# Kernel optimization log

Measured on AMD Instinct MI355X. Metric: run time of the kernel, lower is better.

Reference implementation:

```python
import jax, jax.numpy as jnp
import numpy as np

BS, S, DM, H, DK, DV, PRED = 64, 128, 512, 8, 512, 512, 96
NF = S * DM  # Flatten_Head nf = patch_num * d_model
SCALE_INIT = (DM // H) ** (-0.5)  # head_dim from d_model//n_heads per _ScaledDotProductAttention


def setup_inputs() -> dict:
    key = jax.random.key(0)
    ks = jax.random.split(key, 24)
    g = lambda k, shp: (0.02 * jax.random.normal(k, shp)).astype(jnp.float32)
    inp = {
        "x": jax.random.normal(ks[0], (BS, S, DM), dtype=jnp.float32),
        "prev": jax.random.normal(ks[1], (BS, H, S, S), dtype=jnp.float32),
        # multi-head attention projections (d_k = d_v = d_model per TMBlock)
        "Wq": g(ks[2], (DM, H * DK)), "bq": jnp.zeros((H * DK,), jnp.float32),
        "Wk": g(ks[3], (DM, H * DK)), "bk": jnp.zeros((H * DK,), jnp.float32),
        "Wv": g(ks[4], (DM, H * DV)), "bv": jnp.zeros((H * DV,), jnp.float32),
        "Wo": g(ks[5], (H * DV, DM)), "bo": jnp.zeros((DM,), jnp.float32),
        "scale": jnp.float32(SCALE_INIT),
        # InterPatchMixing: Linear(PatchNum, PatchNum) x2
        "Wi1": g(ks[6], (S, S)), "bi1": jnp.zeros((S,), jnp.float32),
        "Wi2": g(ks[7], (S, S)), "bi2": jnp.zeros((S,), jnp.float32),
        # IntraPatchMixing: Linear(PatchEmbedDim, PatchEmbedDim) x2
        "Wt1": g(ks[8], (DM, DM)), "bt1": jnp.zeros((DM,), jnp.float32),
        "Wt2": g(ks[9], (DM, DM)), "bt2": jnp.zeros((DM,), jnp.float32),
        # Flatten_Head (non-individual): Linear(nf, pred_len)
        "Wh": g(ks[10], (NF, PRED)), "bh": jnp.zeros((PRED,), jnp.float32),
    }
    return inp


def reference(x, prev, Wq, bq, Wk, bk, Wv, bv, Wo, bo, scale,
              Wi1, bi1, Wi2, bi2, Wt1, bt1, Wt2, bt2, Wh, bh):
    bs = x.shape[0]
    # projections -> [bs, H, S, d]
    q = (x @ Wq + bq).reshape(bs, S, H, DK).transpose(0, 2, 1, 3)
    k = (x @ Wk + bk).reshape(bs, S, H, DK).transpose(0, 2, 1, 3)
    v = (x @ Wv + bv).reshape(bs, S, H, DV).transpose(0, 2, 1, 3)
    # manual scaled dot-product attention with residual attention bias (Realformer)
    scores = jnp.einsum('bhqd,bhkd->bhqk', q, k) * scale + prev
    attn = jax.nn.softmax(scores, axis=-1)  # dropout is identity at eval
    o = jnp.einsum('bhqk,bhkd->bhqd', attn, v)
    o = o.transpose(0, 2, 1, 3).reshape(bs, S, H * DV)
    o = o @ Wo + bo  # [bs, S, DM]
    # InterPatchMixing over the patch axis (last dim must be PatchNum)
    t = o.transpose(0, 2, 1)  # [bs, DM, S]
    t = jax.nn.relu(t @ Wi1 + bi1) @ Wi2 + bi2
    y = t.transpose(0, 2, 1)  # [bs, S, DM]
    # IntraPatchMixing over embed dim
    z = jax.nn.relu(y @ Wt1 + bt1) @ Wt2 + bt2
    # Flatten_Head: flatten last two dims -> Linear(nf, pred_len)
    out = z.reshape(bs, NF) @ Wh + bh  # [bs, PRED]
    return out
```

## Files before the change

kernel.cpp:

```cpp
#include <hip/hip_runtime.h>
#include <cstdint>
#include <cstddef>

typedef __bf16 bf16_t;
typedef __bf16 bf16x8 __attribute__((ext_vector_type(8)));
typedef __bf16 bf16x4 __attribute__((ext_vector_type(4)));
typedef float  f32x4  __attribute__((ext_vector_type(4)));

#define MFMA(a, b, c) __builtin_amdgcn_mfma_f32_16x16x32_bf16((a), (b), (c), 0, 0, 0)

__device__ __forceinline__ void gload16(const bf16_t* g, bf16_t* l) {
  __builtin_amdgcn_global_load_lds(
      (const __attribute__((address_space(1))) void*)g,
      (__attribute__((address_space(3))) void*)l, 16, 0, 0);
}


__global__ __launch_bounds__(256) void k_convert_dual(const float* __restrict__ in,
                                                      bf16_t* __restrict__ xb,
                                                      bf16_t* __restrict__ xT) {
  __shared__ bf16_t tile[32][34];
  int tx = threadIdx.x & 31, ty = threadIdx.x >> 5;
  int c0 = blockIdx.x * 32, r0 = blockIdx.y * 32;
#pragma unroll
  for (int j = 0; j < 4; ++j) {
    int r = r0 + ty + j * 8;
    bf16_t bv = (bf16_t)in[(size_t)r * 512 + c0 + tx];
    xb[(size_t)r * 512 + c0 + tx] = bv;
    tile[ty + j * 8][tx] = bv;
  }
  __syncthreads();
  int b = (r0 + tx) >> 7, s = (r0 + tx) & 127;
#pragma unroll
  for (int j = 0; j < 4; ++j) {
    int i = c0 + ty + j * 8;
    xT[(size_t)b * 65536 + (size_t)i * 128 + s] = tile[tx][ty + j * 8];
  }
}

__global__ __launch_bounds__(256) void k_transpose_convert(const float* __restrict__ in,
                                                           bf16_t* __restrict__ out,
                                                           int R, int C) {
  __shared__ float tile[32][33];
  int tx = threadIdx.x & 31, ty = threadIdx.x >> 5;
  int c0 = blockIdx.x * 32, r0 = blockIdx.y * 32;
#pragma unroll
  for (int j = 0; j < 4; ++j)
    tile[ty + j * 8][tx] = in[(size_t)(r0 + ty + j * 8) * C + c0 + tx];
  __syncthreads();
#pragma unroll
  for (int j = 0; j < 4; ++j)
    out[(size_t)(c0 + ty + j * 8) * R + r0 + tx] = (bf16_t)tile[tx][ty + j * 8];
}

__global__ __launch_bounds__(256) void k_transpose_b16(const bf16_t* __restrict__ in,
                                                       bf16_t* __restrict__ out,
                                                       int R, int C) {
  __shared__ bf16_t tile[32][34];
  size_t base = (size_t)blockIdx.z * R * C;
  int tx = threadIdx.x & 31, ty = threadIdx.x >> 5;
  int c0 = blockIdx.x * 32, r0 = blockIdx.y * 32;
#pragma unroll
  for (int j = 0; j < 4; ++j)
    tile[ty + j * 8][tx] = in[base + (size_t)(r0 + ty + j * 8) * C + c0 + tx];
  __syncthreads();
#pragma unroll
  for (int j = 0; j < 4; ++j)
    out[base + (size_t)(c0 + ty + j * 8) * R + r0 + tx] = tile[tx][ty + j * 8];
}

template <int BMODE>
__global__ __launch_bounds__(256) void k_wprod(const float* __restrict__ Ap,
                                               const float* __restrict__ Bp,
                                               bf16_t* __restrict__ out,
                                               int ldA, int ldB) {
  __shared__ __align__(16) bf16_t S[128 * 68 * 2];
  bf16_t* As = S;
  bf16_t* Bs = S + 128 * 68;
  const int tid = threadIdx.x, lane = tid & 63, wave = tid >> 6;
  const int wr = (wave >> 1) * 64, wc = (wave & 1) * 64;
  const int lr = lane & 15, lk = (lane >> 4) * 8, frow = (lane >> 4) * 4;
  const int m0 = blockIdx.x * 128, n0 = blockIdx.y * 128, h = blockIdx.z;
  const int sr = tid >> 3, sc = (tid & 7) * 8;
  f32x4 acc[4][4] = {};

  for (int kt = 0; kt < 512; kt += 64) {
#pragma unroll
    for (int rr = 0; rr < 4; ++rr) {
      int r = sr + 32 * rr;
      const float* ap = Ap + (size_t)(m0 + r) * ldA + h * 512 + kt + sc;
      bf16x8 av;
#pragma unroll
      for (int e = 0; e < 8; ++e) av[e] = (bf16_t)ap[e];
      *(bf16x8*)(As + r * 68 + sc) = av;
    }
    if (BMODE == 0) {
#pragma unroll
      for (int rr = 0; rr < 4; ++rr) {
        int r = sr + 32 * rr;
        const float* bp = Bp + (size_t)(n0 + r) * ldB + h * 512 + kt + sc;
        bf16x8 bv;
#pragma unroll
        for (int e = 0; e < 8; ++e) bv[e] = (bf16_t)bp[e];
        *(bf16x8*)(Bs + r * 68 + sc) = bv;
      }
    } else {
#pragma unroll
      for (int rr = 0; rr < 8; ++rr) {
        int kr = (tid >> 5) + 8 * rr;
        int nc = (tid & 31) * 4;
        const float* bp = Bp + (size_t)(h * 512 + kt + kr) * ldB + n0 + nc;
        float4 v = *(const float4*)bp;
        Bs[(nc + 0) * 68 + kr] = (bf16_t)v.x;
        Bs[(nc + 1) * 68 + kr] = (bf16_t)v.y;
        Bs[(nc + 2) * 68 + kr] = (bf16_t)v.z;
        Bs[(nc + 3) * 68 + kr] = (bf16_t)v.w;
      }
    }
    __syncthreads();
#pragma unroll
    for (int kk = 0; kk < 2; ++kk) {
      bf16x8 af[4], bfr[4];
#pragma unroll
      for (int i = 0; i < 4; ++i)
        af[i] = *(const bf16x8*)(As + (wr + i * 16 + lr) * 68 + kk * 32 + lk);
#pragma unroll
      for (int j = 0; j < 4; ++j)
        bfr[j] = *(const bf16x8*)(Bs + (wc + j * 16 + lr) * 68 + kk * 32 + lk);
#pragma unroll
      for (int i = 0; i < 4; ++i)
#pragma unroll
        for (int j = 0; j < 4; ++j)
          acc[i][j] = MFMA(af[i], bfr[j], acc[i][j]);
    }
    __syncthreads();
  }

  bf16_t* Full = S;
#pragma unroll
  for (int i = 0; i < 4; ++i)
#pragma unroll
    for (int j = 0; j < 4; ++j)
#pragma unroll
      for (int q = 0; q < 4; ++q)
        Full[(wc + j * 16 + lr) * 136 + wr + i * 16 + frow + q] = (bf16_t)acc[i][j][q];
  __syncthreads();
#pragma unroll
  for (int it = 0; it < 8; ++it) {
    int r = it * 16 + (tid >> 4);
    int c = (tid & 15) * 8;
    *(bf16x8*)(out + ((size_t)(h * 512 + n0 + r)) * 512 + m0 + c) =
        *(const bf16x8*)(Full + r * 136 + c);
  }
}

__global__ __launch_bounds__(256) void k_sbias2(const float* __restrict__ Wq,
                                                const float* __restrict__ bk,
                                                const float* __restrict__ Wk,
                                                const float* __restrict__ bq,
                                                bf16_t* __restrict__ W12b,
                                                float* __restrict__ c) {
  const int lane = threadIdx.x & 63, wave = threadIdx.x >> 6;
  const int i = blockIdx.x * 4 + wave;
  for (int h = 0; h < 8; ++h) {
    float s1 = 0.f, s2 = 0.f;
    for (int d = lane; d < 512; d += 64) {
      s1 += Wq[(size_t)i * 4096 + h * 512 + d] * bk[h * 512 + d];
      s2 += Wk[(size_t)i * 4096 + h * 512 + d] * bq[h * 512 + d];
    }
#pragma unroll
    for (int o = 32; o > 0; o >>= 1) { s1 += __shfl_down(s1, o); s2 += __shfl_down(s2, o); }
    if (lane == 0) {
      W12b[h * 512 + i] = (bf16_t)s1;
      W12b[(8 + h) * 512 + i] = (bf16_t)s2;
    }
  }
  if (blockIdx.x == 0 && wave == 0) {
    for (int h = 0; h < 8; ++h) {
      float cc = 0.f;
      for (int d = lane; d < 512; d += 64) cc += bq[h * 512 + d] * bk[h * 512 + d];
#pragma unroll
      for (int o = 32; o > 0; o >>= 1) cc += __shfl_down(cc, o);
      if (lane == 0) c[h] = cc;
    }
  }
}

__global__ __launch_bounds__(256) void k_tbias2(const bf16_t* __restrict__ xb,
                                                const bf16_t* __restrict__ W12b,
                                                const float* __restrict__ cb,
                                                float* __restrict__ TallT) {
  __shared__ __align__(16) bf16_t Ws[16 * 516];
  const int tid = threadIdx.x, lane = tid & 63, wave = tid >> 6;
  const int lr = lane & 15, lk = (lane >> 4) * 8, frow = (lane >> 4) * 4;
  for (int i = tid; i < 1024; i += 256) {
    int r = i >> 6, ccol = (i & 63) * 8;
    *(bf16x8*)(Ws + r * 516 + ccol) = *(const bf16x8*)(W12b + r * 512 + ccol);
  }
  __syncthreads();
  const int row0 = blockIdx.x * 64 + wave * 16;
  const bf16_t* xr = xb + (size_t)(row0 + lr) * 512 + lk;
  f32x4 acc = {};
#pragma unroll
  for (int kx = 0; kx < 16; ++kx) {
    bf16x8 af = *(const bf16x8*)(xr + kx * 32);
    bf16x8 bfv = *(const bf16x8*)(Ws + lr * 516 + kx * 32 + lk);
    acc = MFMA(af, bfv, acc);
  }
#pragma unroll
  for (int q = 0; q < 4; ++q) {
    int r = row0 + frow + q;
    float v = acc[q] + (lr < 8 ? cb[lr] : 0.f);
    TallT[(size_t)lr * 8192 + r] = v;
  }
}

__global__ __launch_bounds__(256) void k_cvec1(const float* __restrict__ bv,
                                               const float* __restrict__ Wo,
                                               float* __restrict__ cpart) {
  int cch = blockIdx.x, d = threadIdx.x * 2;
  float ax = 0.f, ay = 0.f;
  for (int n = cch * 128; n < cch * 128 + 128; ++n) {
    float b = bv[n];
    float2 w = *(const float2*)(Wo + (size_t)n * 512 + d);
    ax += b * w.x; ay += b * w.y;
  }
  cpart[(size_t)cch * 512 + d] = ax;
  cpart[(size_t)cch * 512 + d + 1] = ay;
}
__global__ __launch_bounds__(256) void k_cvec2(const float* __restrict__ cpart,
                                               const float* __restrict__ bo,
                                               float* __restrict__ cvec) {
  int d = blockIdx.x * 256 + threadIdx.x;
  float s = bo[d];
  for (int cch = 0; cch < 32; ++cch) s += cpart[(size_t)cch * 512 + d];
  cvec[d] = s;
}

__global__ __launch_bounds__(64, 2) void k_attn9(const bf16_t* __restrict__ xb,
                                                 const bf16_t* __restrict__ xT,
                                                 bf16_t* __restrict__ TU,
                                                 const float* __restrict__ prev,
                                                 const float* __restrict__ scale_p,
                                                 const float* __restrict__ TallT,
                                                 int hg) {
  __shared__ __align__(16) bf16_t Pl[16 * 136];
  __shared__ __align__(16) bf16_t Bw[16 * 72];

  const int lane = threadIdx.x;
  const int lr = lane & 15, lk = (lane >> 4) * 8, frow = (lane >> 4) * 4;
  const int bid = blockIdx.x;
  const int bx = (bid & 7) * 256 + (bid >> 3);
  const int b = bx >> 5, hp = (bx >> 3) & 3, rg = bx & 7;
  const int h = hg * 4 + hp;
  const int r0 = rg * 16;
  const bf16_t* xB = xb + (size_t)b * 65536;
  const bf16_t* xTB = xT + (size_t)b * 65536;
  bf16_t* tB = TU + ((size_t)hp * 8192 + b * 128 + r0) * 512;

  bf16x8 tf[16];
  const bf16_t* aP = tB + (size_t)lr * 512 + lk;
#pragma unroll
  for (int kx = 0; kx < 16; ++kx) tf[kx] = *(const bf16x8*)(aP + kx * 32);

  f32x4 sacc[8] = {};
  const bf16_t* bP = xB + (size_t)lr * 512 + lk;
#pragma unroll
  for (int kc = 0; kc < 8; ++kc) {
    bf16x8 bb0[8], bb1[8];
#pragma unroll
    for (int j = 0; j < 8; ++j)
      bb0[j] = *(const bf16x8*)(bP + (size_t)j * 8192 + (2 * kc) * 32);
#pragma unroll
    for (int j = 0; j < 8; ++j)
      bb1[j] = *(const bf16x8*)(bP + (size_t)j * 8192 + (2 * kc + 1) * 32);
    __builtin_amdgcn_s_setprio(1);
#pragma unroll
    for (int j = 0; j < 8; ++j) sacc[j] = MFMA(tf[2 * kc], bb0[j], sacc[j]);
#pragma unroll
    for (int j = 0; j < 8; ++j) sacc[j] = MFMA(tf[2 * kc + 1], bb1[j], sacc[j]);
    __builtin_amdgcn_s_setprio(0);
  }

  const float scl = scale_p[0];
  const float* t1p = TallT + h * 8192 + b * 128 + r0;
  const float* t2p = TallT + (8 + h) * 8192 + b * 128;
  float t2r[8];
#pragma unroll
  for (int j = 0; j < 8; ++j) t2r[j] = t2p[j * 16 + lr];
#pragma unroll
  for (int e = 0; e < 4; ++e) {
    const int rl = frow + e;
    const float t1 = t1p[rl];
    const float* prow = prev + (((size_t)(b * 8 + h)) * 128 + r0 + rl) * 128;
    float pv[8];
#pragma unroll
    for (int j = 0; j < 8; ++j) pv[j] = prow[j * 16 + lr];
    float mx = -3.4e38f;
#pragma unroll
    for (int j = 0; j < 8; ++j) {
      float v = scl * (sacc[j][e] + t1 + t2r[j]) + pv[j];
      sacc[j][e] = v;
      mx = fmaxf(mx, v);
    }
    mx = fmaxf(mx, __shfl_xor(mx, 1));
    mx = fmaxf(mx, __shfl_xor(mx, 2));
    mx = fmaxf(mx, __shfl_xor(mx, 4));
    mx = fmaxf(mx, __shfl_xor(mx, 8));
    float sum = 0.f;
#pragma unroll
    for (int j = 0; j < 8; ++j) {
      float p = __expf(sacc[j][e] - mx);
      sacc[j][e] = p;
      sum += p;
    }
    sum += __shfl_xor(sum, 1);
    sum += __shfl_xor(sum, 2);
    sum += __shfl_xor(sum, 4);
    sum += __shfl_xor(sum, 8);
    float inv = 1.f / sum;
#pragma unroll
    for (int j = 0; j < 8; ++j)
      Pl[rl * 136 + j * 16 + lr] = (bf16_t)(sacc[j][e] * inv);
  }

#pragma unroll
  for (int dc = 0; dc < 8; ++dc) {
    bf16x8 xf[16];
#pragma unroll
    for (int kk = 0; kk < 4; ++kk)
#pragma unroll
      for (int j = 0; j < 4; ++j)
        xf[kk * 4 + j] =
            *(const bf16x8*)(xTB + (size_t)(dc * 64 + j * 16 + lr) * 128 + kk * 32 + lk);
    f32x4 oacc[4] = {};
    __builtin_amdgcn_s_setprio(1);
#pragma unroll
    for (int kk = 0; kk < 4; ++kk) {
      bf16x8 pa = *(const bf16x8*)(Pl + lr * 136 + kk * 32 + lk);
#pragma unroll
      for (int j = 0; j < 4; ++j) oacc[j] = MFMA(pa, xf[kk * 4 + j], oacc[j]);
    }
    __builtin_amdgcn_s_setprio(0);
#pragma unroll
    for (int j = 0; j < 4; ++j)
#pragma unroll
      for (int e = 0; e < 4; ++e)
        Bw[(frow + e) * 72 + j * 16 + lr] = (bf16_t)oacc[j][e];
#pragma unroll
    for (int r2 = 0; r2 < 2; ++r2) {
      int row = lane >> 2, chunk = (lane & 3) + r2 * 4;
      *(bf16x8*)(tB + (size_t)row * 512 + dc * 64 + chunk * 8) =
          *(const bf16x8*)(Bw + row * 72 + chunk * 8);
    }
  }
}

template <int OUTMODE, int RELU>
__global__ __launch_bounds__(256) void k_gemm(const bf16_t* __restrict__ A,
                                              const bf16_t* __restrict__ Bt,
                                              const float* __restrict__ bias,
                                              bf16_t* __restrict__ C,
                                              int M, int N, int K) {
  __shared__ __align__(16) bf16_t As[128 * 64];
  __shared__ __align__(16) bf16_t Bs[128 * 64];
  const int tid = threadIdx.x, lane = tid & 63, wave = tid >> 6;
  const int wr = (wave >> 1) * 64, wc = (wave & 1) * 64;
  const int m0 = blockIdx.x * 128, n0 = blockIdx.y * 128;
  const int lr = lane & 15, lk = (lane >> 4) * 8, frow = (lane >> 4) * 4;
  const int grow = lane >> 3;
  const int gcol = ((lane & 7) ^ grow) * 8;
  const int rmask = (lr & 7) << 3;
  f32x4 acc[4][4] = {};

  for (int kt = 0; kt < K; kt += 64) {
#pragma unroll
    for (int i = 0; i < 4; ++i) {
      int t = wave * 4 + i;
      int row = t * 8 + grow;
      gload16(A + (size_t)(m0 + row) * K + kt + gcol, As + t * 512);
      gload16(Bt + (size_t)(n0 + row) * K + kt + gcol, Bs + t * 512);
    }
    __syncthreads();
#pragma unroll
    for (int kk = 0; kk < 2; ++kk) {
      const int col = (kk * 32 + lk) ^ rmask;
      bf16x8 af[4], bfr[4];
#pragma unroll
      for (int i = 0; i < 4; ++i)
        af[i] = *(const bf16x8*)(As + (wr + i * 16 + lr) * 64 + col);
#pragma unroll
      for (int j = 0; j < 4; ++j)
        bfr[j] = *(const bf16x8*)(Bs + (wc + j * 16 + lr) * 64 + col);
#pragma unroll
      for (int i = 0; i < 4; ++i)
#pragma unroll
        for (int j = 0; j < 4; ++j)
          acc[i][j] = MFMA(af[i], bfr[j], acc[i][j]);
    }
    __syncthreads();
  }
#pragma unroll
  for (int j = 0; j < 4; ++j) {
    int gn = n0 + wc + j * 16 + lr;
    float bv = bias ? bias[gn] : 0.0f;
#pragma unroll
    for (int i = 0; i < 4; ++i) {
#pragma unroll
      for (int q = 0; q < 4; ++q) {
        int gm = m0 + wr + i * 16 + frow + q;
        float v = acc[i][j][q] + bv;
        if (RELU) v = v > 0.0f ? v : 0.0f;
        if (OUTMODE == 0)
          C[(size_t)gm * N + gn] = (bf16_t)v;
        else
          C[((size_t)(gn >> 9) * 8192 + gm) * 512 + (gn & 511)] = (bf16_t)v;
      }
    }
  }
}

template <int RELU>
__global__ __launch_bounds__(256) void k_gemm64(const bf16_t* __restrict__ A,
                                                const bf16_t* __restrict__ Bt,
                                                const float* __restrict__ bias,
                                                bf16_t* __restrict__ C,
                                                int M, int N, int K) {
  __shared__ __align__(16) bf16_t As[64 * 68];
  __shared__ __align__(16) bf16_t Bs[128 * 68];
  const int tid = threadIdx.x, lane = tid & 63, wave = tid >> 6;
  const int m0 = blockIdx.x * 64, n0 = blockIdx.y * 128;
  const int lr = lane & 15, lk = (lane >> 4) * 8, frow = (lane >> 4) * 4;
  const int sr = tid >> 3, sc = (tid & 7) * 8;
  f32x4 acc[8] = {};

  for (int kt = 0; kt < K; kt += 64) {
#pragma unroll
    for (int i = 0; i < 2; ++i) {
      int r = i * 32 + sr;
      *(bf16x8*)(As + r * 68 + sc) = *(const bf16x8*)(A + (size_t)(m0 + r) * K + kt + sc);
    }
#pragma unroll
    for (int i = 0; i < 4; ++i) {
      int r = i * 32 + sr;
      *(bf16x8*)(Bs + r * 68 + sc) = *(const bf16x8*)(Bt + (size_t)(n0 + r) * K + kt + sc);
    }
    __syncthreads();
#pragma unroll
    for (int kk = 0; kk < 2; ++kk) {
      bf16x8 af = *(const bf16x8*)(As + (wave * 16 + lr) * 68 + kk * 32 + lk);
      bf16x8 bfr[8];
#pragma unroll
      for (int j = 0; j < 8; ++j)
        bfr[j] = *(const bf16x8*)(Bs + (j * 16 + lr) * 68 + kk * 32 + lk);
#pragma unroll
      for (int j = 0; j < 8; ++j) acc[j] = MFMA(af, bfr[j], acc[j]);
    }
    __syncthreads();
  }
#pragma unroll
  for (int j = 0; j < 8; ++j) {
    int gn = n0 + j * 16 + lr;
    float bv = bias ? bias[gn] : 0.0f;
#pragma unroll
    for (int q = 0; q < 4; ++q) {
      int gm = m0 + wave * 16 + frow + q;
      float v = acc[j][q] + bv;
      if (RELU) v = v > 0.0f ? v : 0.0f;
      C[(size_t)gm * N + gn] = (bf16_t)v;
    }
  }
}

template <int MODE>
__global__ __launch_bounds__(256) void k_gemm2n(const bf16_t* __restrict__ U,
                                                const bf16_t* __restrict__ bt2,
                                                float* __restrict__ o1acc,
                                                const float* __restrict__ cvec,
                                                bf16_t* __restrict__ o1b, int g) {
  __shared__ __align__(16) bf16_t As[128 * 64];
  __shared__ __align__(16) bf16_t Bs[64 * 64];
  const int tid = threadIdx.x, lane = tid & 63, wave = tid >> 6;
  const int wr = (wave >> 1) * 64, wc = (wave & 1) * 32;
  const int m0 = blockIdx.x * 128, n0 = blockIdx.y * 64;
  const int lr = lane & 15, lk = (lane >> 4) * 8, frow = (lane >> 4) * 4;
  const int grow = lane >> 3;
  const int gcol = ((lane & 7) ^ grow) * 8;
  const int rmask = (lr & 7) << 3;
  f32x4 acc[4][2] = {};

  for (int kt = 0; kt < 2048; kt += 64) {
    const int slab = kt >> 9, off = kt & 511;
#pragma unroll
    for (int i = 0; i < 4; ++i) {
      int t = wave * 4 + i;
      int row = t * 8 + grow;
      gload16(U + ((size_t)slab * 8192 + m0 + row) * 512 + off + gcol, As + t * 512);
    }
#pragma unroll
    for (int i = 0; i < 2; ++i) {
      int t = wave * 2 + i;
      int row = t * 8 + grow;
      gload16(bt2 + ((size_t)(g * 4 + slab) * 512 + n0 + row) * 512 + off + gcol,
              Bs + t * 512);
    }
    __syncthreads();
#pragma unroll
    for (int kk = 0; kk < 2; ++kk) {
      const int col = (kk * 32 + lk) ^ rmask;
      bf16x8 af[4], bfr[2];
#pragma unroll
      for (int i = 0; i < 4; ++i)
        af[i] = *(const bf16x8*)(As + (wr + i * 16 + lr) * 64 + col);
#pragma unroll
      for (int j = 0; j < 2; ++j)
        bfr[j] = *(const bf16x8*)(Bs + (wc + j * 16 + lr) * 64 + col);
#pragma unroll
      for (int i = 0; i < 4; ++i)
#pragma unroll
        for (int j = 0; j < 2; ++j)
          acc[i][j] = MFMA(af[i], bfr[j], acc[i][j]);
    }
    __syncthreads();
  }
#pragma unroll
  for (int j = 0; j < 2; ++j) {
    int gn = n0 + wc + j * 16 + lr;
#pragma unroll
    for (int i = 0; i < 4; ++i) {
#pragma unroll
      for (int q = 0; q < 4; ++q) {
        int gm = m0 + wr + i * 16 + frow + q;
        size_t idx = (size_t)gm * 512 + gn;
        if (MODE == 0)
          o1acc[idx] = acc[i][j][q];
        else
          o1b[idx] = (bf16_t)(acc[i][j][q] + o1acc[idx] + cvec[gn]);
      }
    }
  }
}

__global__ __launch_bounds__(256) void k_head_partial(const bf16_t* __restrict__ Z,
                                                      const bf16_t* __restrict__ WhT,
                                                      float* __restrict__ part) {
  __shared__ __align__(16) bf16_t As[64 * 68];
  __shared__ __align__(16) bf16_t Bs[96 * 68];
  const int tid = threadIdx.x, lane = tid & 63, wave = tid >> 6;
  const int wr = (wave >> 1) * 32, wc = (wave & 1) * 48;
  const int lr = lane & 15, lk = (lane >> 4) * 8, frow = (lane >> 4) * 4;
  const int k0 = blockIdx.x * 256;
  const int sr = tid >> 3, sc = (tid & 7) * 8;
  f32x4 acc[2][3] = {};
  for (int kt = 0; kt < 256; kt += 64) {
#pragma unroll
    for (int i = 0; i < 2; ++i) {
      int r = i * 32 + sr;
      *(bf16x8*)(As + r * 68 + sc) = *(const bf16x8*)(Z + (size_t)r * 65536 + k0 + kt + sc);
    }
#pragma unroll
    for (int i = 0; i < 3; ++i) {
      int r = i * 32 + sr;
      *(bf16x8*)(Bs + r * 68 + sc) = *(const bf16x8*)(WhT + (size_t)r * 65536 + k0 + kt + sc);
    }
    __syncthreads();
#pragma unroll
    for (int kk = 0; kk < 2; ++kk) {
      bf16x8 af[2], bfr[3];
#pragma unroll
      for (int i = 0; i < 2; ++i)
        af[i] = *(const bf16x8*)(As + (wr + i * 16 + lr) * 68 + kk * 32 + lk);
#pragma unroll
      for (int j = 0; j < 3; ++j)
        bfr[j] = *(const bf16x8*)(Bs + (wc + j * 16 + lr) * 68 + kk * 32 + lk);
#pragma unroll
      for (int i = 0; i < 2; ++i)
#pragma unroll
        for (int j = 0; j < 3; ++j)
          acc[i][j] = MFMA(af[i], bfr[j], acc[i][j]);
    }
    __syncthreads();
  }
#pragma unroll
  for (int i = 0; i < 2; ++i)
#pragma unroll
    for (int j = 0; j < 3; ++j)
#pragma unroll
      for (int q = 0; q < 4; ++q) {
        int m = wr + i * 16 + frow + q;
        int n = wc + j * 16 + lr;
        part[(size_t)blockIdx.x * 6144 + m * 96 + n] = acc[i][j][q];
      }
}

__global__ __launch_bounds__(256) void k_head_reduce(const float* __restrict__ part,
                                                     const float* __restrict__ bias,
                                                     float* __restrict__ out) {
  int idx = blockIdx.x * 256 + threadIdx.x;
  if (idx >= 6144) return;
  float s = bias[idx % 96];
  for (int kb = 0; kb < 256; ++kb) s += part[(size_t)kb * 6144 + idx];
  out[idx] = s;
}

__global__ void k_sentinel(float* out, int n, float val) {
  int i = blockIdx.x * 256 + threadIdx.x;
  if (i < n) out[i] = val;
}

extern "C" void kernel_launch(void* const* d_in, const int* in_sizes, int n_in,
                              void* d_out, int out_size, void* d_ws, size_t ws_size,
                              hipStream_t stream) {
  const float* x    = (const float*)d_in[0];
  const float* prev = (const float*)d_in[1];
  const float* Wq = (const float*)d_in[2];   const float* bq = (const float*)d_in[3];
  const float* Wk = (const float*)d_in[4];   const float* bk = (const float*)d_in[5];
  const float* Wv = (const float*)d_in[6];   const float* bv = (const float*)d_in[7];
  const float* Wo = (const float*)d_in[8];   const float* bo = (const float*)d_in[9];
  const float* scale = (const float*)d_in[10];
  const float* Wi1 = (const float*)d_in[11]; const float* bi1 = (const float*)d_in[12];
  const float* Wi2 = (const float*)d_in[13]; const float* bi2 = (const float*)d_in[14];
  const float* Wt1 = (const float*)d_in[15]; const float* bt1w = (const float*)d_in[16];
  const float* Wt2 = (const float*)d_in[17]; const float* bt2w = (const float*)d_in[18];
  const float* Wh = (const float*)d_in[19];  const float* bh = (const float*)d_in[20];
  float* out = (float*)d_out;

  char* p = (char*)d_ws;
  auto carve = [&](size_t bytes) {
    char* r = p;
    p += (bytes + 255) & ~(size_t)255;
    return r;
  };
  bf16_t* xb    = (bf16_t*)carve((size_t)8192 * 512 * 2);
  bf16_t* xTo1b = (bf16_t*)carve((size_t)8192 * 512 * 2);
  float*  o1acc = (float*)carve((size_t)8192 * 512 * 4);
  bf16_t* bt1   = (bf16_t*)carve((size_t)4096 * 512 * 2);
  bf16_t* bt2   = (bf16_t*)carve((size_t)4096 * 512 * 2);
  bf16_t* W12b  = (bf16_t*)carve(16 * 512 * 2);
  float*  cb    = (float*)carve(8 * 4);
  float*  cvec  = (float*)carve(512 * 4);
  char*   arena = carve((size_t)8192 * 2048 * 2);
  bf16_t* TU    = (bf16_t*)arena;
  float*  cpart = (float*)arena;
  bf16_t* xT    = xTo1b;
  bf16_t* o1b   = xTo1b;
  float*  TallT = (float*)bt1;
  char* q2 = arena;
  auto carve2 = [&](size_t bytes) {
    char* r = q2;
    q2 += (bytes + 255) & ~(size_t)255;
    return r;
  };
  bf16_t* whT  = (bf16_t*)carve2((size_t)96 * 65536 * 2);
  bf16_t* wt1T = (bf16_t*)carve2((size_t)512 * 512 * 2);
  bf16_t* wt2T = (bf16_t*)carve2((size_t)512 * 512 * 2);
  bf16_t* wi1T = (bf16_t*)carve2((size_t)128 * 128 * 2);
  bf16_t* wi2T = (bf16_t*)carve2((size_t)128 * 128 * 2);
  float*  hp   = (float*)carve2((size_t)256 * 64 * 96 * 4);
  bf16_t* bufB = (bf16_t*)carve2((size_t)8192 * 512 * 2);

  if ((size_t)(p - (char*)d_ws) > ws_size) {
    k_sentinel<<<24, 256, 0, stream>>>(out, 6144, (float)ws_size);
    return;
  }

  dim3 blk(256);
  k_cvec1<<<32, blk, 0, stream>>>(bv, Wo, cpart);
  k_cvec2<<<2, blk, 0, stream>>>(cpart, bo, cvec);
  k_convert_dual<<<dim3(16, 256), blk, 0, stream>>>(x, xb, xT);
  k_wprod<0><<<dim3(4, 4, 8), blk, 0, stream>>>(Wq, Wk, bt1, 4096, 4096);
  k_wprod<1><<<dim3(4, 4, 8), blk, 0, stream>>>(Wv, Wo, bt2, 4096, 512);
  k_sbias2<<<128, blk, 0, stream>>>(Wq, bk, Wk, bq, W12b, cb);

  k_gemm<2, 0><<<dim3(64, 16), blk, 0, stream>>>(xb, bt1, nullptr, TU, 8192, 2048, 512);
  k_tbias2<<<128, blk, 0, stream>>>(xb, W12b, cb, TallT);
  k_attn9<<<2048, dim3(64), 0, stream>>>(xb, xT, TU, prev, scale, TallT, 0);
  k_gemm2n<0><<<dim3(64, 8), blk, 0, stream>>>(TU, bt2, o1acc, cvec, o1b, 0);
  k_gemm<2, 0><<<dim3(64, 16), blk, 0, stream>>>(xb, bt1 + (size_t)2048 * 512, nullptr, TU,
                                                 8192, 2048, 512);
  k_attn9<<<2048, dim3(64), 0, stream>>>(xb, xT, TU, prev, scale, TallT, 1);
  k_gemm2n<1><<<dim3(64, 8), blk, 0, stream>>>(TU, bt2, o1acc, cvec, o1b, 1);

  k_transpose_convert<<<dim3(4, 4), blk, 0, stream>>>(Wi1, wi1T, 128, 128);
  k_transpose_convert<<<dim3(4, 4), blk, 0, stream>>>(Wi2, wi2T, 128, 128);
  k_transpose_convert<<<dim3(16, 16), blk, 0, stream>>>(Wt1, wt1T, 512, 512);
  k_transpose_convert<<<dim3(16, 16), blk, 0, stream>>>(Wt2, wt2T, 512, 512);
  k_transpose_convert<<<dim3(3, 2048), blk, 0, stream>>>(Wh, whT, 65536, 96);

  k_transpose_b16<<<dim3(16, 4, 64), blk, 0, stream>>>(o1b, bufB, 128, 512);
  k_gemm64<1><<<dim3(512, 1), blk, 0, stream>>>(bufB, wi1T, bi1, o1b, 32768, 128, 128);
  k_gemm64<0><<<dim3(512, 1), blk, 0, stream>>>(o1b, wi2T, bi2, bufB, 32768, 128, 128);
  k_transpose_b16<<<dim3(4, 16, 64), blk, 0, stream>>>(bufB, o1b, 512, 128);

  k_gemm64<1><<<dim3(128, 4), blk, 0, stream>>>(o1b, wt1T, bt1w, bufB, 8192, 512, 512);
  k_gemm64<0><<<dim3(128, 4), blk, 0, stream>>>(bufB, wt2T, bt2w, o1b, 8192, 512, 512);

  k_head_partial<<<256, blk, 0, stream>>>(o1b, whT, hp);
  k_head_reduce<<<24, blk, 0, stream>>>(hp, bh, out);
}
```

Measured before the change: 462.4 us.

## Add 4-wave attention kernel sharing x tiles across heads in LDS for first head group

Introduces k_attn10, where one 256-thread block handles four heads (one per wave) for the same batch and row group. The x and xT tiles are staged once in LDS and shared by all four waves, where k_attn9 ran one 64-thread block per head and loaded them separately. The aim is to cut redundant global and LDS traffic and raise occupancy. The cost is more barriers per block, and only the first head-group launch is switched, so the second still uses k_attn9.

Measured after the change: 474.6 us. 2.6% more time.

```diff
diff --git a/kernel.cpp b/kernel.cpp
--- a/kernel.cpp
+++ b/kernel.cpp
@@ -353,6 +353,133 @@
       *(bf16x8*)(tB + (size_t)row * 512 + dc * 64 + chunk * 8) =
           *(const bf16x8*)(Bw + row * 72 + chunk * 8);
     }
+  }
+}
+
+__global__ __launch_bounds__(256, 2) void k_attn10(const bf16_t* __restrict__ xb,
+                                                   const bf16_t* __restrict__ xT,
+                                                   bf16_t* __restrict__ TU,
+                                                   const float* __restrict__ prev,
+                                                   const float* __restrict__ scale_p,
+                                                   const float* __restrict__ TallT,
+                                                   int hg) {
+  __shared__ __align__(16) bf16_t XsXt[8448];
+  __shared__ __align__(16) bf16_t Pl[4][16 * 136];
+  __shared__ __align__(16) bf16_t Bw[4][16 * 72];
+
+  const int tid = threadIdx.x, lane = tid & 63, wave = tid >> 6;
+  const int lr = lane & 15, lk = (lane >> 4) * 8, frow = (lane >> 4) * 4;
+  const int bid = blockIdx.x;
+  const int bx = (bid & 7) * 64 + (bid >> 3);
+  const int b = bx >> 3, rg = bx & 7;
+  const int h = hg * 4 + wave;
+  const int r0 = rg * 16;
+  const bf16_t* xB = xb + (size_t)b * 65536;
+  const bf16_t* xTB = xT + (size_t)b * 65536;
+  bf16_t* tB = TU + ((size_t)wave * 8192 + b * 128 + r0) * 512;
+
+  bf16x8 tf[16];
+  const bf16_t* aP = tB + (size_t)lr * 512 + lk;
+#pragma unroll
+  for (int kx = 0; kx < 16; ++kx) tf[kx] = *(const bf16x8*)(aP + kx * 32);
+
+  f32x4 sacc[8] = {};
+  bf16_t* Xs = XsXt;
+  const int srow = tid >> 4, sc0 = (tid & 15) * 32;
+  for (int j = 0; j < 8; ++j) {
+#pragma unroll
+    for (int e = 0; e < 4; ++e)
+      *(bf16x8*)(Xs + srow * 516 + sc0 + e * 8) =
+          *(const bf16x8*)(xB + (size_t)(j * 16 + srow) * 512 + sc0 + e * 8);
+    __syncthreads();
+    __builtin_amdgcn_s_setprio(1);
+#pragma unroll
+    for (int kx = 0; kx < 16; ++kx) {
+      bf16x8 bfv = *(const bf16x8*)(Xs + lr * 516 + kx * 32 + lk);
+      sacc[j] = MFMA(tf[kx], bfv, sacc[j]);
+    }
+    __builtin_amdgcn_s_setprio(0);
+    __syncthreads();
+  }
+
+  const float scl = scale_p[0];
+  const float* t1p = TallT + h * 8192 + b * 128 + r0;
+  const float* t2p = TallT + (8 + h) * 8192 + b * 128;
+  bf16_t* Plw = Pl[wave];
+  float t2r[8];
+#pragma unroll
+  for (int j = 0; j < 8; ++j) t2r[j] = t2p[j * 16 + lr];
+#pragma unroll
+  for (int e = 0; e < 4; ++e) {
+    const int rl = frow + e;
+    const float t1 = t1p[rl];
+    const float* prow = prev + (((size_t)(b * 8 + h)) * 128 + r0 + rl) * 128;
+    float pv[8];
+#pragma unroll
+    for (int j = 0; j < 8; ++j) pv[j] = prow[j * 16 + lr];
+    float mx = -3.4e38f;
+#pragma unroll
+    for (int j = 0; j < 8; ++j) {
+      float v = scl * (sacc[j][e] + t1 + t2r[j]) + pv[j];
+      sacc[j][e] = v;
+      mx = fmaxf(mx, v);
+    }
+    mx = fmaxf(mx, __shfl_xor(mx, 1));
+    mx = fmaxf(mx, __shfl_xor(mx, 2));
+    mx = fmaxf(mx, __shfl_xor(mx, 4));
+    mx = fmaxf(mx, __shfl_xor(mx, 8));
+    float sum = 0.f;
+#pragma unroll
+    for (int j = 0; j < 8; ++j) {
+      float p = __expf(sacc[j][e] - mx);
+      sacc[j][e] = p;
+      sum += p;
+    }
+    sum += __shfl_xor(sum, 1);
+    sum += __shfl_xor(sum, 2);
+    sum += __shfl_xor(sum, 4);
+    sum += __shfl_xor(sum, 8);
+    float inv = 1.f / sum;
+#pragma unroll
+    for (int j = 0; j < 8; ++j)
+      Plw[rl * 136 + j * 16 + lr] = (bf16_t)(sacc[j][e] * inv);
+  }
+  __syncthreads();
+
+  bf16_t* Xt = XsXt;
+  bf16_t* Bww = Bw[wave];
+  const int trow = tid >> 2, tc0 = (tid & 3) * 32;
+  for (int dc = 0; dc < 8; ++dc) {
+#pragma unroll
+    for (int e = 0; e < 4; ++e)
+      *(bf16x8*)(Xt + trow * 132 + tc0 + e * 8) =
+          *(const bf16x8*)(xTB + (size_t)(dc * 64 + trow) * 128 + tc0 + e * 8);
+    __syncthreads();
+    f32x4 oacc[4] = {};
+    __builtin_amdgcn_s_setprio(1);
+#pragma unroll
+    for (int kk = 0; kk < 4; ++kk) {
+      bf16x8 pa = *(const bf16x8*)(Plw + lr * 136 + kk * 32 + lk);
+      bf16x8 xf[4];
+#pragma unroll
+      for (int j = 0; j < 4; ++j)
+        xf[j] = *(const bf16x8*)(Xt + (j * 16 + lr) * 132 + kk * 32 + lk);
+#pragma unroll
+      for (int j = 0; j < 4; ++j) oacc[j] = MFMA(pa, xf[j], oacc[j]);
+    }
+    __builtin_amdgcn_s_setprio(0);
+#pragma unroll
+    for (int j = 0; j < 4; ++j)
+#pragma unroll
+      for (int e = 0; e < 4; ++e)
+        Bww[(frow + e) * 72 + j * 16 + lr] = (bf16_t)oacc[j][e];
+#pragma unroll
+    for (int r2 = 0; r2 < 2; ++r2) {
+      int row = lane >> 2, chunk = (lane & 3) + r2 * 4;
+      *(bf16x8*)(tB + (size_t)row * 512 + dc * 64 + chunk * 8) =
+          *(const bf16x8*)(Bww + row * 72 + chunk * 8);
+    }
+    __syncthreads();
   }
 }
 
@@ -674,7 +801,7 @@
 
   k_gemm<2, 0><<<dim3(64, 16), blk, 0, stream>>>(xb, bt1, nullptr, TU, 8192, 2048, 512);
   k_tbias2<<<128, blk, 0, stream>>>(xb, W12b, cb, TallT);
-  k_attn9<<<2048, dim3(64), 0, stream>>>(xb, xT, TU, prev, scale, TallT, 0);
+  k_attn10<<<512, blk, 0, stream>>>(xb, xT, TU, prev, scale, TallT, 0);
   k_gemm2n<0><<<dim3(64, 8), blk, 0, stream>>>(TU, bt2, o1acc, cvec, o1b, 0);
   k_gemm<2, 0><<<dim3(64, 16), blk, 0, stream>>>(xb, bt1 + (size_t)2048 * 512, nullptr, TU,
                                                  8192, 2048, 512);
```
